# Performance work log

Hardware: AMD Instinct MI355X
Metric: run time of the kernel (lower is better)

Reference implementation:

```python
import jax, jax.numpy as jnp
import numpy as np

NARROW = 127.0                      # narrow int8 range [-127, 127]
ACT_SCALE = 6.0 / 127.0             # fixed stand-in for learned ActQuant per-tensor scale
FLOW_SCALE = 3.96875 / 127.0        # ConstFlowQuant: max_val 3.96875, 8-bit narrow


def ste_round(x):
    # straight-through rounding (Brevitas-style)
    return x + jax.lax.stop_gradient(jnp.round(x) - x)


def act_quant(x, scale):
    # per-tensor narrow int8 fake-quant (quantize -> clamp -> dequantize)
    return scale * jnp.clip(ste_round(x / scale), -NARROW, NARROW)


def weight_quant(w):
    # per-tensor stats-based narrow int8 weight fake-quant
    s = jax.lax.stop_gradient(jnp.max(jnp.abs(w))) / NARROW + 1e-12
    return s * jnp.clip(ste_round(w / s), -NARROW, NARROW)


def conv2d(x, w, b, groups=1, pad=0):
    y = jax.lax.conv_general_dilated(
        x, w, window_strides=(1, 1), padding=[(pad, pad), (pad, pad)],
        dimension_numbers=("NCHW", "OIHW", "NCHW"), feature_group_count=groups)
    return y + b[None, :, None, None]


def setup_inputs() -> dict:
    key = jax.random.key(0)
    ks = jax.random.split(key, 12)
    B, H, W = 8, 120, 160
    cor_planes = 4 * (2 * 3 + 1) ** 2  # 196
    return {
        "flow": jax.random.normal(ks[0], (B, 2, H, W), jnp.float32),
        "corr": jax.random.normal(ks[1], (B, cor_planes, H, W), jnp.float32),
        "Wc1": jax.random.normal(ks[2], (96, cor_planes, 1, 1), jnp.float32) * 0.05,
        "bc1": jax.random.normal(ks[3], (96,), jnp.float32) * 0.05,
        "Wf1": jax.random.normal(ks[4], (64, 2, 1, 1), jnp.float32) * 0.05,
        "bf1": jax.random.normal(ks[5], (64,), jnp.float32) * 0.05,
        "Wf2": jax.random.normal(ks[6], (32, 64, 1, 1), jnp.float32) * 0.05,
        "bf2": jax.random.normal(ks[7], (32,), jnp.float32) * 0.05,
        "Wd": jax.random.normal(ks[8], (128, 1, 3, 3), jnp.float32) * 0.05,
        "bd": jax.random.normal(ks[9], (128,), jnp.float32) * 0.05,
        "Wp": jax.random.normal(ks[10], (80, 128, 1, 1), jnp.float32) * 0.05,
        "bp": jax.random.normal(ks[11], (80,), jnp.float32) * 0.05,
    }


def reference(flow, corr, Wc1, bc1, Wf1, bf1, Wf2, bf2, Wd, bd, Wp, bp):
    # convc1: 1x1 quant conv with output ActQuant, then ReLU
    cor = jax.nn.relu(act_quant(conv2d(corr, weight_quant(Wc1), bc1), ACT_SCALE))
    # convf1: 1x1 quant conv (no output quant), ReLU
    flo = jax.nn.relu(conv2d(flow, weight_quant(Wf1), bf1))
    # convf2: input ActQuant, 1x1 conv, output quant (shared with convc1), ReLU
    flo = jax.nn.relu(act_quant(conv2d(act_quant(flo, ACT_SCALE), weight_quant(Wf2), bf2), ACT_SCALE))
    # QuantCat with ConstFlowQuant on inputs and output -> [B,128,H,W]
    cor_flo = act_quant(
        jnp.concatenate([act_quant(cor, FLOW_SCALE), act_quant(flo, FLOW_SCALE)], axis=1),
        FLOW_SCALE)
    # depthwise 3x3 quant conv (groups=128), input ActQuant
    d = conv2d(act_quant(cor_flo, ACT_SCALE), weight_quant(Wd), bd, groups=128, pad=1)
    # pointwise 1x1 quant conv, input ActQuant, ReLU
    out = jax.nn.relu(conv2d(act_quant(d, ACT_SCALE), weight_quant(Wp), bp))
    # final QuantCat(out, flow) with ConstFlowQuant -> [B,82,H,W]
    return act_quant(
        jnp.concatenate([act_quant(out, FLOW_SCALE), act_quant(flow, FLOW_SCALE)], axis=1),
        FLOW_SCALE)
```

## Files before the change

kernel.cpp:

```cpp
#include <hip/hip_runtime.h>
#include <hip/hip_bf16.h>
#include <cstddef>

#define BB   8
#define HH   120
#define WW   160
#define HW   19200
#define NPIX 153600
#define CORC 196

#define AS_  ((float)(6.0/127.0))
#define FS_  0.03125f

#define OFF_WF1 18832
#define OFF_WF2 18960
#define OFF_WD  21008
#define OFF_WPQ_US 44320
#define CFQ_BYTE_OFF 131072

typedef __attribute__((ext_vector_type(8)))  short short8;
typedef __attribute__((ext_vector_type(4)))  float f32x4;
typedef unsigned int u32;

__device__ __forceinline__ float clip127(float x) {
    return fminf(fmaxf(x, -127.f), 127.f);
}

__device__ __forceinline__ unsigned short f2bf(float x) {
    unsigned int u = __float_as_uint(x);
    unsigned int r = (u + 0x7fffu + ((u >> 16) & 1u)) >> 16;
    return (unsigned short)r;
}

__global__ __launch_bounds__(256) void quant_weights(
    const float* __restrict__ Wc1, const float* __restrict__ Wf1,
    const float* __restrict__ Wf2, const float* __restrict__ Wd,
    const float* __restrict__ Wp,  float* __restrict__ ws)
{
    __shared__ float red[256];
    const int t = blockIdx.x;
    const float* src = (t == 0) ? Wc1 : (t == 1) ? Wf1 : (t == 2) ? Wf2 : (t == 3) ? Wd : Wp;
    const int n = (t == 0) ? 18816 : (t == 1) ? 128 : (t == 2) ? 2048 : (t == 3) ? 1152 : 10240;
    const int tid = threadIdx.x;

    float m = 0.f;
    for (int i = tid; i < n; i += 256) m = fmaxf(m, fabsf(src[i]));
    red[tid] = m;
    __syncthreads();
    for (int s = 128; s > 0; s >>= 1) {
        if (tid < s) red[tid] = fmaxf(red[tid], red[tid + s]);
        __syncthreads();
    }
    const float s = red[0] / 127.0f + 1e-12f;

    if (t == 0) {
        unsigned short* bf = (unsigned short*)ws + 32;
        for (int j = tid; j < 21504; j += 256) {
            const int e    = j & 7;
            const int l    = (j >> 3) & 63;
            const int tile = j >> 9;
            const int nt   = tile % 6;
            const int kt   = tile / 6;
            const int out  = nt * 16 + (l & 15);
            const int k    = kt * 32 + ((l >> 4) << 3) + e;
            float q = 0.f;
            if (k < 196) q = clip127(rintf(Wc1[out * 196 + k] / s));
            bf[j] = f2bf(q);
        }
        if (tid == 0) ws[2] = s;
    } else if (t == 4) {
        unsigned short* bf = (unsigned short*)ws + OFF_WPQ_US;
        for (int j = tid; j < 10240; j += 256) {
            const int e    = j & 7;
            const int l    = (j >> 3) & 63;
            const int tile = j >> 9;
            const int nt   = tile % 5;
            const int kt   = tile / 5;
            const int o    = nt * 16 + (l & 15);
            const int k    = kt * 32 + ((l >> 4) << 3) + e;
            const float q  = clip127(rintf(Wp[o * 128 + k] / s));
            bf[j] = f2bf(q);
        }
        if (tid == 0) ws[1] = s;
    } else {
        for (int i = tid; i < n; i += 256) {
            const float q = clip127(rintf(src[i] / s));
            if (t == 1) {
                ws[OFF_WF1 + i] = s * q;
            } else if (t == 2) {
                int o = i / 64, c = i % 64;
                ws[OFF_WF2 + c * 32 + o] = s * q;
            } else {
                ws[OFF_WD + i] = q;
            }
        }
        if (tid == 0 && t == 3) ws[0] = s;
    }
}

#define NSLAB 5
#define SLAB_B 8192
#define CSTR 256
#define TS8  68
__global__ __launch_bounds__(256, 3) void k1_convc1(
    const float* __restrict__ corr, const float* __restrict__ bc1,
    const float* __restrict__ ws,   signed char* __restrict__ cfq)
{
    __shared__ __align__(1024) char smem[NSLAB * SLAB_B];

    const int tid  = threadIdx.x;
    const int w    = tid >> 6;
    const int l    = tid & 63;
    const int bid  = blockIdx.x;
    const int wgid = (bid & 7) * 300 + (bid >> 3);
    const int p0   = wgid * 64;
    const int b    = p0 / HW;
    const int hw0  = p0 % HW;
    const float* cp = corr + (size_t)b * CORC * HW + hw0;

    const short8* Bfr = (const short8*)((const unsigned short*)ws + 32);
    const int nbase = (w & 1) * 3;

#define DECLB(KT)                                                              \
    const short8 b##KT##_0 = Bfr[((KT) * 6 + nbase + 0) * 64 + l];             \
    const short8 b##KT##_1 = Bfr[((KT) * 6 + nbase + 1) * 64 + l];             \
    const short8 b##KT##_2 = Bfr[((KT) * 6 + nbase + 2) * 64 + l];
    DECLB(0) DECLB(1) DECLB(2) DECLB(3) DECLB(4) DECLB(5) DECLB(6)
#undef DECLB
    __builtin_amdgcn_sched_barrier(0);

#define STAGE(KT)                                                                     \
    {   char* dbase = smem + ((KT) % NSLAB) * SLAB_B;                                 \
        _Pragma("unroll")                                                             \
        for (int i = 0; i < 2; ++i) {                                                 \
            const int cg = w * 2 + i;                            \
            int chl = (KT) * 32 + cg * 4 + (l >> 4);                                  \
            chl = chl < CORC ? chl : (CORC - 1);                                      \
            const char* src = (const char*)cp + (size_t)chl * (HW * 4)                \
                              + (l & 15) * 16;                                        \
            u32* dst = (u32*)(dbase + cg * 1024);                                     \
            __builtin_amdgcn_global_load_lds(                                         \
                (const __attribute__((address_space(1))) u32*)src,                    \
                (__attribute__((address_space(3))) u32*)dst, 16, 0, 0);               \
        }                                                                             }

    STAGE(0) STAGE(1) STAGE(2) STAGE(3) STAGE(4)

    const int pixoff = ((w >> 1) * 32 + (l & 15)) * 4;
    const int chbase = (l >> 4) << 3;

    f32x4 ac00 = {0.f,0.f,0.f,0.f}, ac01 = ac00, ac02 = ac00;
    f32x4 ac10 = ac00, ac11 = ac00, ac12 = ac00;

#define MF(BB_, A0, A1)                                                          \
        A0 = __builtin_amdgcn_mfma_f32_16x16x32_bf16(l0_, BB_, A0, 0, 0, 0);     \
        A0 = __builtin_amdgcn_mfma_f32_16x16x32_bf16(h0_, BB_, A0, 0, 0, 0);     \
        A1 = __builtin_amdgcn_mfma_f32_16x16x32_bf16(l1_, BB_, A1, 0, 0, 0);     \
        A1 = __builtin_amdgcn_mfma_f32_16x16x32_bf16(h1_, BB_, A1, 0, 0, 0);

#define KSTEP(KT, WN)                                                             \
    {   asm volatile("s_waitcnt vmcnt(" #WN ")" ::: "memory");                    \
        __builtin_amdgcn_sched_barrier(0);                                        \
        __builtin_amdgcn_s_barrier();                         \
        __builtin_amdgcn_sched_barrier(0);                                        \
        const char* abase = smem + ((KT) % NSLAB) * SLAB_B;                       \
        float v0[8], v1[8];                                                       \
        _Pragma("unroll")                                                         \
        for (int e = 0; e < 8; ++e) {                                             \
            const char* ap = abase + (chbase + e) * CSTR + pixoff;                \
            v0[e] = *(const float*)ap;                                            \
            v1[e] = *(const float*)(ap + 64);                                     \
        }                                                                         \
        __builtin_amdgcn_sched_barrier(0);                                        \
        asm volatile("s_waitcnt lgkmcnt(0)" ::: "memory");                        \
        __builtin_amdgcn_sched_barrier(0);                                        \
        __builtin_amdgcn_s_barrier();                          \
        __builtin_amdgcn_sched_barrier(0);                                        \
        if ((KT) + NSLAB < 7) STAGE((KT) + NSLAB)                                 \
        __builtin_amdgcn_sched_barrier(0);                                        \
        short8 h0_, l0_, h1_, l1_;                                                \
        _Pragma("unroll")                                                         \
        for (int e = 0; e < 8; ++e) {                                             \
            const float va = v0[e], vb = v1[e];                                   \
            const unsigned short ha = f2bf(va);                                   \
            const unsigned short hb = f2bf(vb);                                   \
            h0_[e] = (short)ha; h1_[e] = (short)hb;                               \
            l0_[e] = (short)f2bf(va - __uint_as_float((unsigned int)ha << 16));   \
            l1_[e] = (short)f2bf(vb - __uint_as_float((unsigned int)hb << 16));   \
        }                                                                         \
        MF(b##KT##_0, ac00, ac10) MF(b##KT##_1, ac01, ac11)                       \
        MF(b##KT##_2, ac02, ac12)                                                 }

    KSTEP(0, 8) KSTEP(1, 8) KSTEP(2, 8) KSTEP(3, 6)
    KSTEP(4, 4) KSTEP(5, 2) KSTEP(6, 0)
#undef KSTEP
#undef MF
#undef STAGE

    const float sc1 = ws[2];
    signed char* t8 = (signed char*)smem;

#define EPI(ACC, NT, TILE)                                                        \
    {   const int out = (nbase + (NT)) * 16 + (l & 15);                           \
        const float bias = bc1[out];                                              \
        _Pragma("unroll")                                                         \
        for (int i = 0; i < 4; ++i) {                                             \
            const int prow = (w >> 1) * 32 + (TILE) * 16 + ((l >> 4) << 2) + i;   \
            float v  = fmaf(sc1, ACC[i], bias);                                   \
            float aq = AS_ * clip127(rintf(v / AS_));                             \
            float r  = fmaxf(aq, 0.f);                                            \
            float kk = fminf(rintf(r * 32.f), 127.f);                             \
            float cf = kk * FS_;                                                  \
            float q8 = clip127(rintf(cf / AS_));                                  \
            t8[out * TS8 + prow] = (signed char)(int)q8;                          \
        }                                                                         }
    EPI(ac00, 0, 0) EPI(ac01, 1, 0) EPI(ac02, 2, 0)
    EPI(ac10, 0, 1) EPI(ac11, 1, 1) EPI(ac12, 2, 1)
#undef EPI
    __syncthreads();

#pragma unroll
    for (int r = 0; r < 6; ++r) {
        const int d   = r * 256 + tid;
        const int out = d >> 4;
        const int pd  = d & 15;
        const u32 v = *(const u32*)(t8 + out * TS8 + pd * 4);
        *(u32*)(cfq + (size_t)(b * 128 + out) * HW + hw0 + pd * 4) = v;
    }
}

typedef __attribute__((ext_vector_type(16))) float f32x16;
__global__ __launch_bounds__(256) void k1_flo(
    const float* __restrict__ flow, const float* __restrict__ bf1,
    const float* __restrict__ bf2,  const float* __restrict__ ws,
    signed char* __restrict__ cfq)
{
    const int p  = blockIdx.x * 256 + threadIdx.x;
    const int b  = p / HW;
    const int hw = p % HW;

    const float f0 = flow[(size_t)(b * 2) * HW + hw];
    const float f1 = flow[(size_t)(b * 2 + 1) * HW + hw];

    f32x16 a2a, a2b;
#pragma unroll
    for (int j = 0; j < 16; ++j) { a2a[j] = 0.f; a2b[j] = 0.f; }

    for (int c = 0; c < 64; ++c) {
        const float w0 = ws[OFF_WF1 + 2 * c];
        const float w1 = ws[OFF_WF1 + 2 * c + 1];
        float v  = fmaf(f0, w0, fmaf(f1, w1, bf1[c]));
        float r  = fmaxf(v, 0.f);
        float af = AS_ * fminf(rintf(r / AS_), 127.f);
        const float* w2 = ws + OFF_WF2 + c * 32;
#pragma unroll
        for (int j = 0; j < 16; ++j) {
            a2a[j] = fmaf(af, w2[j],      a2a[j]);
            a2b[j] = fmaf(af, w2[16 + j], a2b[j]);
        }
    }

    signed char* op = cfq + (size_t)b * 128 * HW + (size_t)96 * HW + hw;
#define FLOEPI(ACC, BASE)                                                        \
    _Pragma("unroll")                                                            \
    for (int j = 0; j < 16; ++j) {                                               \
        const int o = (BASE) + j;                                                \
        float v  = ACC[j] + bf2[o];                                              \
        float aq = AS_ * clip127(rintf(v / AS_));                                \
        float r  = fmaxf(aq, 0.f);                                               \
        float kk = fminf(rintf(r * 32.f), 127.f);                                \
        float cf = kk * FS_;                                                     \
        float q8 = clip127(rintf(cf / AS_));                                     \
        op[(size_t)o * HW] = (signed char)(int)q8;                               \
    }
    FLOEPI(a2a, 0) FLOEPI(a2b, 16)
#undef FLOEPI
}

#define STG_STRIDE 44
__global__ __launch_bounds__(256) void k2_dwpw(
    const float* __restrict__ flow, const float* __restrict__ bd,
    const float* __restrict__ bp,   const float* __restrict__ ws,
    const signed char* __restrict__ cfq, float* __restrict__ out)
{
    __shared__ signed char stage[4 * 128 * STG_STRIDE];
    __shared__ unsigned short afrag[64 * 136];

    const int tid = threadIdx.x;
    const int bid = blockIdx.x;
    const int b   = bid / 300;
    const int rem = bid % 300;
    const int h0  = (rem / 5) * 2;
    const int w0  = (rem % 5) * 32;

    for (int j = tid; j < 5120; j += 256) {
        const int i   = j % 10;
        const int c   = (j / 10) % 128;
        const int row = j / 1280;
        const int h   = h0 - 1 + row;
        const int wb  = w0 - 4 + 4 * i;
        unsigned int v = 0u;
        if (h >= 0 && h < HH && wb >= 0 && wb <= WW - 4)
            v = *(const unsigned int*)(cfq + ((size_t)(b * 128 + c) * HW + (size_t)h * WW + wb));
        *(unsigned int*)(stage + (row * 128 + c) * STG_STRIDE + i * 4) = v;
    }
    __syncthreads();

    const int c0 = tid & 63;
    const int pg = tid >> 6;
    const float sd = ws[0], sp = ws[1];
    const float ASsd = AS_ * sd;

    float wd0[9], wd1[9];
#pragma unroll
    for (int t9 = 0; t9 < 9; ++t9) {
        wd0[t9] = ws[OFF_WD + c0 * 9 + t9];
        wd1[t9] = ws[OFF_WD + (c0 + 64) * 9 + t9];
    }
    const float bd0 = bd[c0], bd1 = bd[c0 + 64];

#pragma unroll
    for (int pp = 0; pp < 16; ++pp) {
        const int pix = pg * 16 + pp;
        const int r   = pix >> 5;
        const int col = pix & 31;
        float s0 = 0.f, s1 = 0.f;
#pragma unroll
        for (int dy = 0; dy < 3; ++dy) {
            const int rb = (r + dy) * 128;
            const int xb = 3 + col;
#pragma unroll
            for (int dd = 0; dd < 3; ++dd) {
                s0 = fmaf((float)stage[(rb + c0     ) * STG_STRIDE + xb + dd], wd0[dy * 3 + dd], s0);
                s1 = fmaf((float)stage[(rb + c0 + 64) * STG_STRIDE + xb + dd], wd1[dy * 3 + dd], s1);
            }
        }
        const float q0 = clip127(rintf(fmaf(ASsd, s0, bd0) / AS_));
        const float q1 = clip127(rintf(fmaf(ASsd, s1, bd1) / AS_));
        afrag[pix * 136 + c0]      = f2bf(q0);
        afrag[pix * 136 + c0 + 64] = f2bf(q1);
    }
    __syncthreads();

    const int wv = tid >> 6;
    const int l  = tid & 63;
    const unsigned short* A = afrag + (size_t)(wv * 16 + (l & 15)) * 136 + ((l >> 4) << 3);
    const short8* Bfr = (const short8*)((const unsigned short*)ws + OFF_WPQ_US);

    f32x4 pc0 = {0.f,0.f,0.f,0.f}, pc1 = pc0, pc2 = pc0, pc3 = pc0, pc4 = pc0;

#define PTSTEP(ACC, KT, NT)                                                      \
    {   short8 bq = Bfr[((KT) * 5 + (NT)) * 64 + l];                             \
        ACC = __builtin_amdgcn_mfma_f32_16x16x32_bf16(a_, bq, ACC, 0, 0, 0);     }
#pragma unroll
    for (int kt = 0; kt < 4; ++kt) {
        short8 a_ = *(const short8*)(A + kt * 32);
        PTSTEP(pc0, kt, 0) PTSTEP(pc1, kt, 1) PTSTEP(pc2, kt, 2)
        PTSTEP(pc3, kt, 3) PTSTEP(pc4, kt, 4)
    }
#undef PTSTEP

    const float ASsp = AS_ * sp;
    float* ob = out + (size_t)b * 82 * HW;

#define PEPI(ACC, NT)                                                            \
    {   const int o = (NT) * 16 + (l & 15);                                      \
        const float bias = bp[o];                                                \
        _Pragma("unroll")                                                        \
        for (int i = 0; i < 4; ++i) {                                            \
            const int pix = wv * 16 + ((l >> 4) << 2) + i;                       \
            const int hw  = (h0 + (pix >> 5)) * WW + w0 + (pix & 31);            \
            float v = fmaf(ASsp, ACC[i], bias);                                  \
            float r = fmaxf(v, 0.f);                                             \
            float k = fminf(rintf(r * 32.f), 127.f);                             \
            ob[(size_t)o * HW + hw] = k * FS_;                                   \
        }                                                                        }
    PEPI(pc0, 0) PEPI(pc1, 1) PEPI(pc2, 2) PEPI(pc3, 3) PEPI(pc4, 4)
#undef PEPI

    if (tid < 128) {
        const int ch  = tid >> 6;
        const int pix = tid & 63;
        const int hw  = (h0 + (pix >> 5)) * WW + w0 + (pix & 31);
        const float f = flow[(size_t)(b * 2 + ch) * HW + hw];
        const float k = clip127(rintf(f * 32.f));
        ob[(size_t)(80 + ch) * HW + hw] = k * FS_;
    }
}

extern "C" void kernel_launch(void* const* d_in, const int* in_sizes, int n_in,
                              void* d_out, int out_size, void* d_ws, size_t ws_size,
                              hipStream_t stream) {
    const float* flow = (const float*)d_in[0];
    const float* corr = (const float*)d_in[1];
    const float* Wc1  = (const float*)d_in[2];
    const float* bc1  = (const float*)d_in[3];
    const float* Wf1  = (const float*)d_in[4];
    const float* bf1  = (const float*)d_in[5];
    const float* Wf2  = (const float*)d_in[6];
    const float* bf2  = (const float*)d_in[7];
    const float* Wd   = (const float*)d_in[8];
    const float* bd   = (const float*)d_in[9];
    const float* Wp   = (const float*)d_in[10];
    const float* bp   = (const float*)d_in[11];

    float* ws = (float*)d_ws;
    signed char* cfq = (signed char*)d_ws + CFQ_BYTE_OFF;
    float* out = (float*)d_out;

    quant_weights<<<5, 256, 0, stream>>>(Wc1, Wf1, Wf2, Wd, Wp, ws);
    k1_convc1<<<NPIX / 64, 256, 0, stream>>>(corr, bc1, ws, cfq);
    k1_flo<<<NPIX / 256, 256, 0, stream>>>(flow, bf1, bf2, ws, cfq);
    k2_dwpw<<<2400, 256, 0, stream>>>(flow, bd, bp, ws, cfq, out);
}
```

Baseline: 163.4 us.

## Fuse flow branch into convc1 kernel and prefetch all K slabs upfront

Removes the separate k1_flo launch by computing the convf1/convf2 flow branch inside k1_convc1, where each wave handles 8 of the 32 output channels for the block's 64 pixels. The work overlaps the corr loads, which are now all 7 slabs issued at kernel start (NSLAB 5→7), removing the mid-loop restaging and one barrier per K step. Divisions by the activation scale are replaced with multiplications by its reciprocal. LDS per block grows to 56KB and occupancy drops to 2 blocks per CU. Multiplying by the reciprocal can occasionally round differently from dividing.

```diff
diff --git a/kernel.cpp b/kernel.cpp
--- a/kernel.cpp
+++ b/kernel.cpp
@@ -10,6 +10,7 @@
 #define CORC 196
 
 #define AS_  ((float)(6.0/127.0))
+#define ASI_ (1.0f / AS_)
 #define FS_  0.03125f
 
 #define OFF_WF1 18832
@@ -98,13 +99,15 @@
     }
 }
 
-#define NSLAB 5
+#define NSLAB 7
 #define SLAB_B 8192
 #define CSTR 256
 #define TS8  68
-__global__ __launch_bounds__(256, 3) void k1_convc1(
-    const float* __restrict__ corr, const float* __restrict__ bc1,
-    const float* __restrict__ ws,   signed char* __restrict__ cfq)
+__global__ __launch_bounds__(256, 2) void k1_convc1(
+    const float* __restrict__ corr, const float* __restrict__ flow,
+    const float* __restrict__ bc1,  const float* __restrict__ bf1,
+    const float* __restrict__ bf2,  const float* __restrict__ ws,
+    signed char* __restrict__ cfq)
 {
     __shared__ __align__(1024) char smem[NSLAB * SLAB_B];
 
@@ -118,6 +121,10 @@
     const int hw0  = p0 % HW;
     const float* cp = corr + (size_t)b * CORC * HW + hw0;
 
+    const float f0 = flow[(size_t)(b * 2) * HW + hw0 + l];
+    const float f1 = flow[(size_t)(b * 2 + 1) * HW + hw0 + l];
+    __builtin_amdgcn_sched_barrier(0);
+
     const short8* Bfr = (const short8*)((const unsigned short*)ws + 32);
     const int nbase = (w & 1) * 3;
 
@@ -130,7 +137,7 @@
     __builtin_amdgcn_sched_barrier(0);
 
 #define STAGE(KT)                                                                     \
-    {   char* dbase = smem + ((KT) % NSLAB) * SLAB_B;                                 \
+    {   char* dbase = smem + (KT) * SLAB_B;                                           \
         _Pragma("unroll")                                                             \
         for (int i = 0; i < 2; ++i) {                                                 \
             const int cg = w * 2 + i;                            \
@@ -144,7 +151,38 @@
                 (__attribute__((address_space(3))) u32*)dst, 16, 0, 0);               \
         }                                                                             }
 
-    STAGE(0) STAGE(1) STAGE(2) STAGE(3) STAGE(4)
+    STAGE(0) STAGE(1) STAGE(2) STAGE(3) STAGE(4) STAGE(5) STAGE(6)
+#undef STAGE
+    __builtin_amdgcn_sched_barrier(0);
+
+    {
+        float a2[8];
+#pragma unroll
+        for (int j = 0; j < 8; ++j) a2[j] = 0.f;
+#pragma unroll 8
+        for (int c = 0; c < 64; ++c) {
+            const float w0 = ws[OFF_WF1 + 2 * c];
+            const float w1 = ws[OFF_WF1 + 2 * c + 1];
+            float v  = fmaf(f0, w0, fmaf(f1, w1, bf1[c]));
+            float r  = fmaxf(v, 0.f);
+            float af = AS_ * fminf(rintf(r * ASI_), 127.f);
+            const float* w2 = ws + OFF_WF2 + c * 32 + w * 8;
+#pragma unroll
+            for (int j = 0; j < 8; ++j) a2[j] = fmaf(af, w2[j], a2[j]);
+        }
+        signed char* op = cfq + (size_t)(b * 128 + 96 + w * 8) * HW + hw0 + l;
+#pragma unroll
+        for (int j = 0; j < 8; ++j) {
+            float v  = a2[j] + bf2[w * 8 + j];
+            float aq = AS_ * clip127(rintf(v * ASI_));
+            float r  = fmaxf(aq, 0.f);
+            float kk = fminf(rintf(r * 32.f), 127.f);
+            float cf = kk * FS_;
+            float q8 = clip127(rintf(cf * ASI_));
+            op[(size_t)j * HW] = (signed char)(int)q8;
+        }
+    }
+    __builtin_amdgcn_sched_barrier(0);
 
     const int pixoff = ((w >> 1) * 32 + (l & 15)) * 4;
     const int chbase = (l >> 4) << 3;
@@ -163,7 +201,7 @@
         __builtin_amdgcn_sched_barrier(0);                                        \
         __builtin_amdgcn_s_barrier();                         \
         __builtin_amdgcn_sched_barrier(0);                                        \
-        const char* abase = smem + ((KT) % NSLAB) * SLAB_B;                       \
+        const char* abase = smem + (KT) * SLAB_B;                                 \
         float v0[8], v1[8];                                                       \
         _Pragma("unroll")                                                         \
         for (int e = 0; e < 8; ++e) {                                             \
@@ -173,10 +211,6 @@
         }                                                                         \
         __builtin_amdgcn_sched_barrier(0);                                        \
         asm volatile("s_waitcnt lgkmcnt(0)" ::: "memory");                        \
-        __builtin_amdgcn_sched_barrier(0);                                        \
-        __builtin_amdgcn_s_barrier();                          \
-        __builtin_amdgcn_sched_barrier(0);                                        \
-        if ((KT) + NSLAB < 7) STAGE((KT) + NSLAB)                                 \
         __builtin_amdgcn_sched_barrier(0);                                        \
         short8 h0_, l0_, h1_, l1_;                                                \
         _Pragma("unroll")                                                         \
@@ -191,11 +225,10 @@
         MF(b##KT##_0, ac00, ac10) MF(b##KT##_1, ac01, ac11)                       \
         MF(b##KT##_2, ac02, ac12)                                                 }
 
-    KSTEP(0, 8) KSTEP(1, 8) KSTEP(2, 8) KSTEP(3, 6)
+    KSTEP(0, 12) KSTEP(1, 10) KSTEP(2, 8) KSTEP(3, 6)
     KSTEP(4, 4) KSTEP(5, 2) KSTEP(6, 0)
 #undef KSTEP
 #undef MF
-#undef STAGE
 
     const float sc1 = ws[2];
     signed char* t8 = (signed char*)smem;
@@ -207,11 +240,11 @@
         for (int i = 0; i < 4; ++i) {                                             \
             const int prow = (w >> 1) * 32 + (TILE) * 16 + ((l >> 4) << 2) + i;   \
             float v  = fmaf(sc1, ACC[i], bias);                                   \
-            float aq = AS_ * clip127(rintf(v / AS_));                             \
+            float aq = AS_ * clip127(rintf(v * ASI_));                            \
             float r  = fmaxf(aq, 0.f);                                            \
             float kk = fminf(rintf(r * 32.f), 127.f);                             \
             float cf = kk * FS_;                                                  \
-            float q8 = clip127(rintf(cf / AS_));                                  \
+            float q8 = clip127(rintf(cf * ASI_));                                 \
             t8[out * TS8 + prow] = (signed char)(int)q8;                          \
         }                                                                         }
     EPI(ac00, 0, 0) EPI(ac01, 1, 0) EPI(ac02, 2, 0)
@@ -227,54 +260,6 @@
         const u32 v = *(const u32*)(t8 + out * TS8 + pd * 4);
         *(u32*)(cfq + (size_t)(b * 128 + out) * HW + hw0 + pd * 4) = v;
     }
-}
-
-typedef __attribute__((ext_vector_type(16))) float f32x16;
-__global__ __launch_bounds__(256) void k1_flo(
-    const float* __restrict__ flow, const float* __restrict__ bf1,
-    const float* __restrict__ bf2,  const float* __restrict__ ws,
-    signed char* __restrict__ cfq)
-{
-    const int p  = blockIdx.x * 256 + threadIdx.x;
-    const int b  = p / HW;
-    const int hw = p % HW;
-
-    const float f0 = flow[(size_t)(b * 2) * HW + hw];
-    const float f1 = flow[(size_t)(b * 2 + 1) * HW + hw];
-
-    f32x16 a2a, a2b;
-#pragma unroll
-    for (int j = 0; j < 16; ++j) { a2a[j] = 0.f; a2b[j] = 0.f; }
-
-    for (int c = 0; c < 64; ++c) {
-        const float w0 = ws[OFF_WF1 + 2 * c];
-        const float w1 = ws[OFF_WF1 + 2 * c + 1];
-        float v  = fmaf(f0, w0, fmaf(f1, w1, bf1[c]));
-        float r  = fmaxf(v, 0.f);
-        float af = AS_ * fminf(rintf(r / AS_), 127.f);
-        const float* w2 = ws + OFF_WF2 + c * 32;
-#pragma unroll
-        for (int j = 0; j < 16; ++j) {
-            a2a[j] = fmaf(af, w2[j],      a2a[j]);
-            a2b[j] = fmaf(af, w2[16 + j], a2b[j]);
-        }
-    }
-
-    signed char* op = cfq + (size_t)b * 128 * HW + (size_t)96 * HW + hw;
-#define FLOEPI(ACC, BASE)                                                        \
-    _Pragma("unroll")                                                            \
-    for (int j = 0; j < 16; ++j) {                                               \
-        const int o = (BASE) + j;                                                \
-        float v  = ACC[j] + bf2[o];                                              \
-        float aq = AS_ * clip127(rintf(v / AS_));                                \
-        float r  = fmaxf(aq, 0.f);                                               \
-        float kk = fminf(rintf(r * 32.f), 127.f);                                \
-        float cf = kk * FS_;                                                     \
-        float q8 = clip127(rintf(cf / AS_));                                     \
-        op[(size_t)o * HW] = (signed char)(int)q8;                               \
-    }
-    FLOEPI(a2a, 0) FLOEPI(a2b, 16)
-#undef FLOEPI
 }
 
 #define STG_STRIDE 44
@@ -335,8 +320,8 @@
                 s1 = fmaf((float)stage[(rb + c0 + 64) * STG_STRIDE + xb + dd], wd1[dy * 3 + dd], s1);
             }
         }
-        const float q0 = clip127(rintf(fmaf(ASsd, s0, bd0) / AS_));
-        const float q1 = clip127(rintf(fmaf(ASsd, s1, bd1) / AS_));
+        const float q0 = clip127(rintf(fmaf(ASsd, s0, bd0) * ASI_));
+        const float q1 = clip127(rintf(fmaf(ASsd, s1, bd1) * ASI_));
         afrag[pix * 136 + c0]      = f2bf(q0);
         afrag[pix * 136 + c0 + 64] = f2bf(q1);
     }
@@ -409,7 +394,6 @@
     float* out = (float*)d_out;
 
     quant_weights<<<5, 256, 0, stream>>>(Wc1, Wf1, Wf2, Wd, Wp, ws);
-    k1_convc1<<<NPIX / 64, 256, 0, stream>>>(corr, bc1, ws, cfq);
-    k1_flo<<<NPIX / 256, 256, 0, stream>>>(flow, bf1, bf2, ws, cfq);
+    k1_convc1<<<NPIX / 64, 256, 0, stream>>>(corr, flow, bc1, bf1, bf2, ws, cfq);
     k2_dwpw<<<2400, 256, 0, stream>>>(flow, bd, bp, ws, cfq, out);
 }
```

After: 168.3 us. 1.03x slower.
